# Kernel optimization log

Hardware: AMD Instinct MI355X
Metric: run time of the kernel (lower is better)

## Reference

```python
import jax, jax.numpy as jnp
import numpy as np

N_NODES = 50000
N_REL = 16
D_EMB = 128
D_HID = 128
D_OUT = 128
N_EDGES = 1600000


def _xavier(key, shape, fan_in, fan_out, dtype=jnp.float32):
    lim = float(np.sqrt(6.0 / (fan_in + fan_out)))
    return jax.random.uniform(key, shape, dtype, -lim, lim)


def setup_inputs() -> dict:
    key = jax.random.key(0)
    ks = jax.random.split(key, 10)
    edge_index = jax.random.randint(ks[0], (2, N_EDGES), 0, N_NODES, dtype=jnp.int64)
    edge_type = jax.random.randint(ks[1], (N_EDGES,), 0, N_REL, dtype=jnp.int64)
    emb = _xavier(ks[2], (N_NODES, D_EMB), N_NODES, D_EMB)
    W1 = _xavier(ks[3], (N_REL, D_EMB, D_HID), D_EMB, D_HID)
    root1 = _xavier(ks[4], (D_EMB, D_HID), D_EMB, D_HID)
    b1 = jnp.zeros((D_HID,), jnp.float32)
    W2 = _xavier(ks[5], (N_REL, D_HID, D_OUT), D_HID, D_OUT)
    root2 = _xavier(ks[6], (D_HID, D_OUT), D_HID, D_OUT)
    b2 = jnp.zeros((D_OUT,), jnp.float32)
    return {"edge_index": edge_index, "edge_type": edge_type, "emb": emb,
            "W1": W1, "root1": root1, "b1": b1,
            "W2": W2, "root2": root2, "b2": b2}


def rgcn_conv(x, edge_index, edge_type, W, W_root, b):
    """PyG RGCNConv (num_bases=None): out_i = x_i @ W_root + b + sum_r mean_{j in N_r(i)} x_j @ W_r.
    Mean-aggregate x_j per (dst, relation) first, then apply relation GEMMs (linearity)."""
    src, dst = edge_index[0], edge_index[1]
    seg = dst * N_REL + edge_type                      # [E] composite (node, rel) key
    x_src = x[src]                                     # [E, d] gather
    summed = jax.ops.segment_sum(x_src, seg, num_segments=N_NODES * N_REL)  # [N*R, d]
    cnt = jax.ops.segment_sum(jnp.ones((src.shape[0],), x.dtype), seg,
                              num_segments=N_NODES * N_REL)                 # [N*R]
    agg = summed / jnp.maximum(cnt, 1.0)[:, None]      # mean; empty (i,r) -> 0
    agg = agg.reshape(N_NODES, N_REL, x.shape[1])      # [N, R, d]
    return jnp.einsum('nrd,rdh->nh', agg, W) + x @ W_root + b


def reference(edge_index, edge_type, emb, W1, root1, b1, W2, root2, b2):
    x = emb                                            # embedding.weight: all-node lookup
    x = jax.nn.relu(rgcn_conv(x, edge_index, edge_type, W1, root1, b1))
    # dropout(p=0.5) omitted: eval-mode identity
    x = rgcn_conv(x, edge_index, edge_type, W2, root2, b2)
    return x
```

## Files before the change

kernel.cpp:

```cpp
#include <hip/hip_runtime.h>

#define N_NODES 50000
#define N_REL 16
#define D 128
#define N_SEG (N_NODES * N_REL)

typedef short bf16x8 __attribute__((ext_vector_type(8)));
typedef float f32x4 __attribute__((ext_vector_type(4)));
typedef unsigned short u16;
typedef unsigned int u32;

__device__ __forceinline__ u16 f32_to_bf16(float f) {
  u32 u = __builtin_bit_cast(u32, f);
  u32 r = (u + 0x7FFFu + ((u >> 16) & 1u)) >> 16;
  return (u16)r;
}
__device__ __forceinline__ float bf16_to_f32(u16 h) {
  u32 u = ((u32)h) << 16;
  return __builtin_bit_cast(float, u);
}

__global__ __launch_bounds__(256) void k_zero4(uint4* __restrict__ p, long long n4) {
  long long i = (long long)blockIdx.x * blockDim.x + threadIdx.x;
  long long stride = (long long)gridDim.x * blockDim.x;
  uint4 z; z.x = z.y = z.z = z.w = 0u;
  for (; i < n4; i += stride) p[i] = z;
}

__global__ __launch_bounds__(256) void k_cvt(const float* __restrict__ in,
                                             u16* __restrict__ out, long long n4) {
  long long i = (long long)blockIdx.x * blockDim.x + threadIdx.x;
  if (i >= n4) return;
  float4 v = ((const float4*)in)[i];
  u32 p0 = (u32)f32_to_bf16(v.x) | ((u32)f32_to_bf16(v.y) << 16);
  u32 p1 = (u32)f32_to_bf16(v.z) | ((u32)f32_to_bf16(v.w) << 16);
  ((u32*)out)[i * 2] = p0;
  ((u32*)out)[i * 2 + 1] = p1;
}

__global__ __launch_bounds__(256) void k_count(const int* __restrict__ dst,
                                               const int* __restrict__ rel,
                                               int* __restrict__ cnt, int E) {
  int e = blockIdx.x * blockDim.x + threadIdx.x;
  if (e < E) atomicAdd(&cnt[dst[e] * N_REL + rel[e]], 1);
}

__global__ __launch_bounds__(256) void k_bsum(const int* __restrict__ cnt,
                                              int* __restrict__ bsum, int n) {
  __shared__ int sm[256];
  int i = blockIdx.x * 256 + threadIdx.x;
  int v = (i < n) ? cnt[i] : 0;
  sm[threadIdx.x] = v;
  __syncthreads();
  for (int s = 128; s > 0; s >>= 1) {
    if (threadIdx.x < s) sm[threadIdx.x] += sm[threadIdx.x + s];
    __syncthreads();
  }
  if (threadIdx.x == 0) bsum[blockIdx.x] = sm[0];
}

__global__ __launch_bounds__(1024) void k_bscan(int* __restrict__ bsum, int nb) {
  __shared__ int sm[1024];
  __shared__ int carry;
  if (threadIdx.x == 0) carry = 0;
  __syncthreads();
  int niter = (nb + 1023) / 1024;
  for (int it = 0; it < niter; ++it) {
    int i = it * 1024 + threadIdx.x;
    int v = (i < nb) ? bsum[i] : 0;
    sm[threadIdx.x] = v;
    __syncthreads();
    for (int s = 1; s < 1024; s <<= 1) {
      int t = (threadIdx.x >= s) ? sm[threadIdx.x - s] : 0;
      __syncthreads();
      sm[threadIdx.x] += t;
      __syncthreads();
    }
    int incl = sm[threadIdx.x];
    int c = carry;
    __syncthreads();
    if (i < nb) bsum[i] = c + incl - v;
    if (threadIdx.x == 1023) carry = c + sm[1023];
    __syncthreads();
  }
}

__global__ __launch_bounds__(256) void k_off(const int* __restrict__ cnt,
                                             const int* __restrict__ bsum,
                                             int* __restrict__ off, int n) {
  __shared__ int sm[256];
  int i = blockIdx.x * 256 + threadIdx.x;
  int v = (i < n) ? cnt[i] : 0;
  sm[threadIdx.x] = v;
  __syncthreads();
  for (int s = 1; s < 256; s <<= 1) {
    int t = (threadIdx.x >= s) ? sm[threadIdx.x - s] : 0;
    __syncthreads();
    sm[threadIdx.x] += t;
    __syncthreads();
  }
  int excl = sm[threadIdx.x] - v + bsum[blockIdx.x];
  if (i < n) off[i] = excl;
  if (i == n - 1) off[n] = excl + v;
}

__global__ __launch_bounds__(256) void k_fill(const int* __restrict__ src,
                                              const int* __restrict__ dst,
                                              const int* __restrict__ rel,
                                              const int* __restrict__ off,
                                              int* __restrict__ cnt,
                                              int* __restrict__ bucket, int E) {
  int e = blockIdx.x * blockDim.x + threadIdx.x;
  if (e >= E) return;
  int seg = dst[e] * N_REL + rel[e];
  int old = atomicSub(&cnt[seg], 1);
  bucket[off[seg] + old - 1] = src[e];
}

__global__ __launch_bounds__(256) void k_wfrag(const float* __restrict__ W,
                                               u16* __restrict__ Wf, int nkb) {
  int tid = blockIdx.x * blockDim.x + threadIdx.x;
  int total = nkb * 8 * 64;
  if (tid >= total) return;
  int lane = tid & 63;
  int t = (tid >> 6) & 7;
  int kb = tid >> 9;
  int h = t * 16 + (lane & 15);
  int kbase = kb * 32 + ((lane >> 4) << 3);
  bf16x8 frag;
#pragma unroll
  for (int j = 0; j < 8; ++j) {
    int k = kbase + j;
    frag[j] = (short)f32_to_bf16(W[(size_t)(k >> 7) * (D * D) + (size_t)(k & 127) * D + h]);
  }
  *(bf16x8*)(Wf + (size_t)tid * 8) = frag;
}

template <int L>
__global__ __launch_bounds__(256) void k_layer(const int* __restrict__ off,
                                               const int* __restrict__ bucket,
                                               const u16* __restrict__ x,
                                               const u16* __restrict__ Wf,
                                               const u16* __restrict__ Rf,
                                               const float* __restrict__ bias,
                                               u16* __restrict__ outb,
                                               float* __restrict__ outf) {
  __shared__ f32x4 red[4][8][64];
  int w = threadIdx.x >> 6;
  int lane = threadIdx.x & 63;
  int node0 = blockIdx.x << 4;
  int m = lane & 15;
  int q = lane >> 4;
  int node = node0 + m;

  f32x4 acc[8];
#pragma unroll
  for (int t = 0; t < 8; ++t)
#pragma unroll
    for (int i = 0; i < 4; ++i) acc[t][i] = 0.0f;

  {
    bf16x8 a = *(const bf16x8*)(x + ((size_t)node << 7) + w * 32 + (q << 3));
    const u16* bp = Rf + ((size_t)w << 12) + ((size_t)lane << 3);
#pragma unroll
    for (int t = 0; t < 8; ++t) {
      bf16x8 b = *(const bf16x8*)(bp + t * 512);
      acc[t] = __builtin_amdgcn_mfma_f32_16x16x32_bf16(a, b, acc[t], 0, 0, 0);
    }
  }

  for (int rr = 0; rr < 4; ++rr) {
    int r = w * 4 + rr;
    int seg = (node << 4) + r;
    int o0 = off[seg];
    int o1 = off[seg + 1];

    float a0[8], a1[8], a2[8], a3[8];
#pragma unroll
    for (int j = 0; j < 8; ++j) { a0[j] = 0.f; a1[j] = 0.f; a2[j] = 0.f; a3[j] = 0.f; }

    for (int i = o0; i < o1; ++i) {
      int s = bucket[i];
      const u16* xs = x + ((size_t)s << 7) + (q << 3);
      bf16x8 v0 = *(const bf16x8*)(xs);
      bf16x8 v1 = *(const bf16x8*)(xs + 32);
      bf16x8 v2 = *(const bf16x8*)(xs + 64);
      bf16x8 v3 = *(const bf16x8*)(xs + 96);
#pragma unroll
      for (int j = 0; j < 8; ++j) {
        a0[j] += bf16_to_f32((u16)v0[j]);
        a1[j] += bf16_to_f32((u16)v1[j]);
        a2[j] += bf16_to_f32((u16)v2[j]);
        a3[j] += bf16_to_f32((u16)v3[j]);
      }
    }

    float sc = (o1 > o0) ? 1.0f / (float)(o1 - o0) : 0.0f;
    bf16x8 f0, f1, f2, f3;
#pragma unroll
    for (int j = 0; j < 8; ++j) {
      f0[j] = (short)f32_to_bf16(a0[j] * sc);
      f1[j] = (short)f32_to_bf16(a1[j] * sc);
      f2[j] = (short)f32_to_bf16(a2[j] * sc);
      f3[j] = (short)f32_to_bf16(a3[j] * sc);
    }

    const u16* bp = Wf + ((size_t)(r * 4) << 12) + ((size_t)lane << 3);
#pragma unroll
    for (int t = 0; t < 8; ++t) {
      bf16x8 b0 = *(const bf16x8*)(bp + t * 512);
      bf16x8 b1 = *(const bf16x8*)(bp + 4096 + t * 512);
      bf16x8 b2 = *(const bf16x8*)(bp + 8192 + t * 512);
      bf16x8 b3 = *(const bf16x8*)(bp + 12288 + t * 512);
      acc[t] = __builtin_amdgcn_mfma_f32_16x16x32_bf16(f0, b0, acc[t], 0, 0, 0);
      acc[t] = __builtin_amdgcn_mfma_f32_16x16x32_bf16(f1, b1, acc[t], 0, 0, 0);
      acc[t] = __builtin_amdgcn_mfma_f32_16x16x32_bf16(f2, b2, acc[t], 0, 0, 0);
      acc[t] = __builtin_amdgcn_mfma_f32_16x16x32_bf16(f3, b3, acc[t], 0, 0, 0);
    }
  }

#pragma unroll
  for (int t = 0; t < 8; ++t) red[w][t][lane] = acc[t];
  __syncthreads();

#pragma unroll
  for (int j = 0; j < 2; ++j) {
    int t = w * 2 + j;
    f32x4 s0 = red[0][t][lane];
    f32x4 s1 = red[1][t][lane];
    f32x4 s2 = red[2][t][lane];
    f32x4 s3 = red[3][t][lane];
    int h = t * 16 + m;
    float bv = bias[h];
#pragma unroll
    for (int r4 = 0; r4 < 4; ++r4) {
      int n = node0 + (q << 2) + r4;
      float v = s0[r4] + s1[r4] + s2[r4] + s3[r4] + bv;
      if (L == 1) {
        v = v > 0.0f ? v : 0.0f;
        outb[(size_t)n * D + h] = f32_to_bf16(v);
      } else {
        outf[(size_t)n * D + h] = v;
      }
    }
  }
}

extern "C" void kernel_launch(void* const* d_in, const int* in_sizes, int n_in,
                              void* d_out, int out_size, void* d_ws, size_t ws_size,
                              hipStream_t stream) {
  const int* edge_index = (const int*)d_in[0];
  const int* edge_type  = (const int*)d_in[1];
  const float* emb   = (const float*)d_in[2];
  const float* W1    = (const float*)d_in[3];
  const float* root1 = (const float*)d_in[4];
  const float* b1    = (const float*)d_in[5];
  const float* W2    = (const float*)d_in[6];
  const float* root2 = (const float*)d_in[7];
  const float* b2    = (const float*)d_in[8];
  float* out = (float*)d_out;

  int E = in_sizes[0] / 2;
  const int* src = edge_index;
  const int* dst = edge_index + E;
  int nblocks_seg = (N_SEG + 255) / 256;

  char* ws = (char*)d_ws;
  size_t off_b = 0;
  auto take = [&](size_t bytes) -> char* {
    char* p = ws + off_b;
    off_b += (bytes + 255) & ~(size_t)255;
    return p;
  };
  int*   cnt    = (int*)take((size_t)N_SEG * 4);
  int*   offs   = (int*)take((size_t)(N_SEG + 1) * 4);
  int*   bsum   = (int*)take((size_t)nblocks_seg * 4);
  int*   bucket = (int*)take((size_t)E * 4);
  u16*   embb   = (u16*)take((size_t)N_NODES * D * 2);
  u16*   x1     = (u16*)take((size_t)N_NODES * D * 2);
  u16*   Wf1    = (u16*)take((size_t)64 * 8 * 512 * 2);
  u16*   Rf1    = (u16*)take((size_t)4 * 8 * 512 * 2);
  u16*   Wf2    = (u16*)take((size_t)64 * 8 * 512 * 2);
  u16*   Rf2    = (u16*)take((size_t)4 * 8 * 512 * 2);

  int eBlocks = (E + 255) / 256;
  int layerBlocks = N_NODES / 16;

  k_zero4<<<512, 256, 0, stream>>>((uint4*)cnt, (long long)N_SEG * 4 / 16);
  k_count<<<eBlocks, 256, 0, stream>>>(dst, edge_type, cnt, E);
  k_bsum<<<nblocks_seg, 256, 0, stream>>>(cnt, bsum, N_SEG);
  k_bscan<<<1, 1024, 0, stream>>>(bsum, nblocks_seg);
  k_off<<<nblocks_seg, 256, 0, stream>>>(cnt, bsum, offs, N_SEG);
  k_fill<<<eBlocks, 256, 0, stream>>>(src, dst, edge_type, offs, cnt, bucket, E);

  k_cvt<<<((N_NODES * D / 4) + 255) / 256, 256, 0, stream>>>(emb, embb,
                                                             (long long)N_NODES * D / 4);
  k_wfrag<<<(64 * 8 * 64 + 255) / 256, 256, 0, stream>>>(W1, Wf1, 64);
  k_wfrag<<<(4 * 8 * 64 + 255) / 256, 256, 0, stream>>>(root1, Rf1, 4);
  k_wfrag<<<(64 * 8 * 64 + 255) / 256, 256, 0, stream>>>(W2, Wf2, 64);
  k_wfrag<<<(4 * 8 * 64 + 255) / 256, 256, 0, stream>>>(root2, Rf2, 4);

  k_layer<1><<<layerBlocks, 256, 0, stream>>>(offs, bucket, embb, Wf1, Rf1, b1,
                                              x1, nullptr);
  k_layer<2><<<layerBlocks, 256, 0, stream>>>(offs, bucket, x1, Wf2, Rf2, b2,
                                              nullptr, out);
}
```

Baseline: 551.2 us.

## Restructure RGCN layer: wave-per-segment gather into LDS, then per-wave output-column MFMA

New measurement: 678.8 us. 1.23x slower.

```diff
diff --git a/kernel.cpp b/kernel.cpp
--- a/kernel.cpp
+++ b/kernel.cpp
@@ -14,10 +14,6 @@
   u32 u = __builtin_bit_cast(u32, f);
   u32 r = (u + 0x7FFFu + ((u >> 16) & 1u)) >> 16;
   return (u16)r;
-}
-__device__ __forceinline__ float bf16_to_f32(u16 h) {
-  u32 u = ((u32)h) << 16;
-  return __builtin_bit_cast(float, u);
 }
 
 __global__ __launch_bounds__(256) void k_zero4(uint4* __restrict__ p, long long n4) {
@@ -137,7 +133,7 @@
 }
 
 template <int L>
-__global__ __launch_bounds__(256) void k_layer(const int* __restrict__ off,
+__global__ __launch_bounds__(512) void k_layer(const int* __restrict__ off,
                                                const int* __restrict__ bucket,
                                                const u16* __restrict__ x,
                                                const u16* __restrict__ Wf,
@@ -145,103 +141,86 @@
                                                const float* __restrict__ bias,
                                                u16* __restrict__ outb,
                                                float* __restrict__ outf) {
-  __shared__ f32x4 red[4][8][64];
-  int w = threadIdx.x >> 6;
-  int lane = threadIdx.x & 63;
+  __shared__ __align__(16) u32 agg[16 * 16 * 64];
+  __shared__ int offs_sm[257];
+  int tid = threadIdx.x;
+  int w = tid >> 6;
+  int lane = tid & 63;
   int node0 = blockIdx.x << 4;
+
+  if (tid < 257) offs_sm[tid] = off[(node0 << 4) + tid];
+  __syncthreads();
+
+  const u32* xw = (const u32*)x;
+
+  for (int k = 0; k < 32; ++k) {
+    int s = (k << 3) | w;
+    int m = s >> 4;
+    int o0 = __builtin_amdgcn_readfirstlane(offs_sm[s]);
+    int o1 = __builtin_amdgcn_readfirstlane(offs_sm[s + 1]);
+    float aL = 0.0f, aH = 0.0f;
+    int i = o0;
+    for (; i + 2 <= o1; i += 2) {
+      int e0 = __builtin_amdgcn_readfirstlane(bucket[i]);
+      int e1 = __builtin_amdgcn_readfirstlane(bucket[i + 1]);
+      u32 v0 = xw[((size_t)e0 << 6) + lane];
+      u32 v1 = xw[((size_t)e1 << 6) + lane];
+      aL += __builtin_bit_cast(float, v0 << 16);
+      aH += __builtin_bit_cast(float, v0 & 0xFFFF0000u);
+      aL += __builtin_bit_cast(float, v1 << 16);
+      aH += __builtin_bit_cast(float, v1 & 0xFFFF0000u);
+    }
+    if (i < o1) {
+      int e0 = __builtin_amdgcn_readfirstlane(bucket[i]);
+      u32 v0 = xw[((size_t)e0 << 6) + lane];
+      aL += __builtin_bit_cast(float, v0 << 16);
+      aH += __builtin_bit_cast(float, v0 & 0xFFFF0000u);
+    }
+    float sc = (o1 > o0) ? 1.0f / (float)(o1 - o0) : 0.0f;
+    u32 p = (u32)f32_to_bf16(aL * sc) | ((u32)f32_to_bf16(aH * sc) << 16);
+    agg[(s << 6) + ((((lane >> 2) ^ m) << 2) | (lane & 3))] = p;
+  }
+  __syncthreads();
+
+  int q = lane >> 4;
   int m = lane & 15;
-  int q = lane >> 4;
-  int node = node0 + m;
-
-  f32x4 acc[8];
-#pragma unroll
-  for (int t = 0; t < 8; ++t)
-#pragma unroll
-    for (int i = 0; i < 4; ++i) acc[t][i] = 0.0f;
+  const u16* aggh = (const u16*)agg;
+
+  f32x4 acc;
+#pragma unroll
+  for (int i = 0; i < 4; ++i) acc[i] = 0.0f;
 
   {
-    bf16x8 a = *(const bf16x8*)(x + ((size_t)node << 7) + w * 32 + (q << 3));
-    const u16* bp = Rf + ((size_t)w << 12) + ((size_t)lane << 3);
-#pragma unroll
-    for (int t = 0; t < 8; ++t) {
-      bf16x8 b = *(const bf16x8*)(bp + t * 512);
-      acc[t] = __builtin_amdgcn_mfma_f32_16x16x32_bf16(a, b, acc[t], 0, 0, 0);
-    }
-  }
-
-  for (int rr = 0; rr < 4; ++rr) {
-    int r = w * 4 + rr;
-    int seg = (node << 4) + r;
-    int o0 = off[seg];
-    int o1 = off[seg + 1];
-
-    float a0[8], a1[8], a2[8], a3[8];
-#pragma unroll
-    for (int j = 0; j < 8; ++j) { a0[j] = 0.f; a1[j] = 0.f; a2[j] = 0.f; a3[j] = 0.f; }
-
-    for (int i = o0; i < o1; ++i) {
-      int s = bucket[i];
-      const u16* xs = x + ((size_t)s << 7) + (q << 3);
-      bf16x8 v0 = *(const bf16x8*)(xs);
-      bf16x8 v1 = *(const bf16x8*)(xs + 32);
-      bf16x8 v2 = *(const bf16x8*)(xs + 64);
-      bf16x8 v3 = *(const bf16x8*)(xs + 96);
-#pragma unroll
-      for (int j = 0; j < 8; ++j) {
-        a0[j] += bf16_to_f32((u16)v0[j]);
-        a1[j] += bf16_to_f32((u16)v1[j]);
-        a2[j] += bf16_to_f32((u16)v2[j]);
-        a3[j] += bf16_to_f32((u16)v3[j]);
-      }
-    }
-
-    float sc = (o1 > o0) ? 1.0f / (float)(o1 - o0) : 0.0f;
-    bf16x8 f0, f1, f2, f3;
-#pragma unroll
-    for (int j = 0; j < 8; ++j) {
-      f0[j] = (short)f32_to_bf16(a0[j] * sc);
-      f1[j] = (short)f32_to_bf16(a1[j] * sc);
-      f2[j] = (short)f32_to_bf16(a2[j] * sc);
-      f3[j] = (short)f32_to_bf16(a3[j] * sc);
-    }
-
-    const u16* bp = Wf + ((size_t)(r * 4) << 12) + ((size_t)lane << 3);
-#pragma unroll
-    for (int t = 0; t < 8; ++t) {
-      bf16x8 b0 = *(const bf16x8*)(bp + t * 512);
-      bf16x8 b1 = *(const bf16x8*)(bp + 4096 + t * 512);
-      bf16x8 b2 = *(const bf16x8*)(bp + 8192 + t * 512);
-      bf16x8 b3 = *(const bf16x8*)(bp + 12288 + t * 512);
-      acc[t] = __builtin_amdgcn_mfma_f32_16x16x32_bf16(f0, b0, acc[t], 0, 0, 0);
-      acc[t] = __builtin_amdgcn_mfma_f32_16x16x32_bf16(f1, b1, acc[t], 0, 0, 0);
-      acc[t] = __builtin_amdgcn_mfma_f32_16x16x32_bf16(f2, b2, acc[t], 0, 0, 0);
-      acc[t] = __builtin_amdgcn_mfma_f32_16x16x32_bf16(f3, b3, acc[t], 0, 0, 0);
-    }
-  }
-
-#pragma unroll
-  for (int t = 0; t < 8; ++t) red[w][t][lane] = acc[t];
-  __syncthreads();
-
-#pragma unroll
-  for (int j = 0; j < 2; ++j) {
-    int t = w * 2 + j;
-    f32x4 s0 = red[0][t][lane];
-    f32x4 s1 = red[1][t][lane];
-    f32x4 s2 = red[2][t][lane];
-    f32x4 s3 = red[3][t][lane];
-    int h = t * 16 + m;
-    float bv = bias[h];
-#pragma unroll
-    for (int r4 = 0; r4 < 4; ++r4) {
-      int n = node0 + (q << 2) + r4;
-      float v = s0[r4] + s1[r4] + s2[r4] + s3[r4] + bv;
-      if (L == 1) {
-        v = v > 0.0f ? v : 0.0f;
-        outb[(size_t)n * D + h] = f32_to_bf16(v);
-      } else {
-        outf[(size_t)n * D + h] = v;
-      }
+    const u16* xr = x + ((size_t)(node0 + m) << 7) + (q << 3);
+#pragma unroll
+    for (int kb = 0; kb < 4; ++kb) {
+      bf16x8 a = *(const bf16x8*)(xr + kb * 32);
+      bf16x8 b = *(const bf16x8*)(Rf + ((((kb << 3) + w) << 9) | (lane << 3)));
+      acc = __builtin_amdgcn_mfma_f32_16x16x32_bf16(a, b, acc, 0, 0, 0);
+    }
+  }
+
+  for (int r = 0; r < 16; ++r) {
+#pragma unroll
+    for (int kb = 0; kb < 4; ++kb) {
+      int c = ((kb << 2) | q) ^ m;
+      bf16x8 a = *(const bf16x8*)(aggh + ((((m << 4) | r) << 7) | (c << 3)));
+      bf16x8 b = *(const bf16x8*)(Wf + (((((r << 2) | kb) << 3) + w) << 9) + (lane << 3));
+      acc = __builtin_amdgcn_mfma_f32_16x16x32_bf16(a, b, acc, 0, 0, 0);
+    }
+  }
+
+  int h = (w << 4) + m;
+  float bv = bias[h];
+#pragma unroll
+  for (int j = 0; j < 4; ++j) {
+    int n = node0 + (q << 2) + j;
+    float v = acc[j] + bv;
+    if (L == 1) {
+      v = v > 0.0f ? v : 0.0f;
+      outb[(size_t)n * D + h] = f32_to_bf16(v);
+    } else {
+      outf[(size_t)n * D + h] = v;
     }
   }
 }
@@ -300,8 +279,8 @@
   k_wfrag<<<(64 * 8 * 64 + 255) / 256, 256, 0, stream>>>(W2, Wf2, 64);
   k_wfrag<<<(4 * 8 * 64 + 255) / 256, 256, 0, stream>>>(root2, Rf2, 4);
 
-  k_layer<1><<<layerBlocks, 256, 0, stream>>>(offs, bucket, embb, Wf1, Rf1, b1,
+  k_layer<1><<<layerBlocks, 512, 0, stream>>>(offs, bucket, embb, Wf1, Rf1, b1,
                                               x1, nullptr);
-  k_layer<2><<<layerBlocks, 256, 0, stream>>>(offs, bucket, x1, Wf2, Rf2, b2,
+  k_layer<2><<<layerBlocks, 512, 0, stream>>>(offs, bucket, x1, Wf2, Rf2, b2,
                                               nullptr, out);
 }
```

## Process two 16-node tiles per block to reuse weight fragments; merge prep kernels

Applied to the files above, without the earlier changes.

Measured after the change: 626.3 us. 13.6% more time.

```diff
diff --git a/kernel.cpp b/kernel.cpp
--- a/kernel.cpp
+++ b/kernel.cpp
@@ -25,17 +25,6 @@
   long long stride = (long long)gridDim.x * blockDim.x;
   uint4 z; z.x = z.y = z.z = z.w = 0u;
   for (; i < n4; i += stride) p[i] = z;
-}
-
-__global__ __launch_bounds__(256) void k_cvt(const float* __restrict__ in,
-                                             u16* __restrict__ out, long long n4) {
-  long long i = (long long)blockIdx.x * blockDim.x + threadIdx.x;
-  if (i >= n4) return;
-  float4 v = ((const float4*)in)[i];
-  u32 p0 = (u32)f32_to_bf16(v.x) | ((u32)f32_to_bf16(v.y) << 16);
-  u32 p1 = (u32)f32_to_bf16(v.z) | ((u32)f32_to_bf16(v.w) << 16);
-  ((u32*)out)[i * 2] = p0;
-  ((u32*)out)[i * 2 + 1] = p1;
 }
 
 __global__ __launch_bounds__(256) void k_count(const int* __restrict__ dst,
@@ -117,11 +106,8 @@
   bucket[off[seg] + old - 1] = src[e];
 }
 
-__global__ __launch_bounds__(256) void k_wfrag(const float* __restrict__ W,
-                                               u16* __restrict__ Wf, int nkb) {
-  int tid = blockIdx.x * blockDim.x + threadIdx.x;
-  int total = nkb * 8 * 64;
-  if (tid >= total) return;
+__device__ __forceinline__ void wfrag_one(const float* __restrict__ W,
+                                          u16* __restrict__ Wf, int tid) {
   int lane = tid & 63;
   int t = (tid >> 6) & 7;
   int kb = tid >> 9;
@@ -136,73 +122,149 @@
   *(bf16x8*)(Wf + (size_t)tid * 8) = frag;
 }
 
+#define CVT_N4 (N_NODES * D / 4)
+#define WF_T (64 * 8 * 64)
+#define RF_T (4 * 8 * 64)
+#define PREP_TOTAL (CVT_N4 + 2 * WF_T + 2 * RF_T)
+
+__global__ __launch_bounds__(256) void k_prep(const float* __restrict__ emb,
+                                              u16* __restrict__ embb,
+                                              const float* __restrict__ W1,
+                                              u16* __restrict__ Wf1,
+                                              const float* __restrict__ W2,
+                                              u16* __restrict__ Wf2,
+                                              const float* __restrict__ R1,
+                                              u16* __restrict__ Rf1,
+                                              const float* __restrict__ R2,
+                                              u16* __restrict__ Rf2) {
+  int tid = blockIdx.x * blockDim.x + threadIdx.x;
+  if (tid < CVT_N4) {
+    float4 v = ((const float4*)emb)[tid];
+    u32 p0 = (u32)f32_to_bf16(v.x) | ((u32)f32_to_bf16(v.y) << 16);
+    u32 p1 = (u32)f32_to_bf16(v.z) | ((u32)f32_to_bf16(v.w) << 16);
+    ((u32*)embb)[tid * 2] = p0;
+    ((u32*)embb)[tid * 2 + 1] = p1;
+    return;
+  }
+  int u = tid - CVT_N4;
+  if (u < WF_T) { wfrag_one(W1, Wf1, u); return; }
+  u -= WF_T;
+  if (u < WF_T) { wfrag_one(W2, Wf2, u); return; }
+  u -= WF_T;
+  if (u < RF_T) { wfrag_one(R1, Rf1, u); return; }
+  u -= RF_T;
+  if (u < RF_T) { wfrag_one(R2, Rf2, u); return; }
+}
+
 template <int L>
-__global__ __launch_bounds__(256) void k_layer(const int* __restrict__ off,
-                                               const int* __restrict__ bucket,
-                                               const u16* __restrict__ x,
-                                               const u16* __restrict__ Wf,
-                                               const u16* __restrict__ Rf,
-                                               const float* __restrict__ bias,
-                                               u16* __restrict__ outb,
-                                               float* __restrict__ outf) {
+__global__ __launch_bounds__(256, 3) void k_layer(const int* __restrict__ off,
+                                                  const int* __restrict__ bucket,
+                                                  const u16* __restrict__ x,
+                                                  const u16* __restrict__ Wf,
+                                                  const u16* __restrict__ Rf,
+                                                  const float* __restrict__ bias,
+                                                  u16* __restrict__ outb,
+                                                  float* __restrict__ outf) {
   __shared__ f32x4 red[4][8][64];
   int w = threadIdx.x >> 6;
   int lane = threadIdx.x & 63;
-  int node0 = blockIdx.x << 4;
+  int node0 = blockIdx.x << 5;
   int m = lane & 15;
   int q = lane >> 4;
-  int node = node0 + m;
-
-  f32x4 acc[8];
+  int nA = node0 + m;
+  bool hasB = (node0 + 16) < N_NODES;
+  int nB = hasB ? (node0 + 16 + m) : nA;
+
+  f32x4 acc0[8], acc1[8];
 #pragma unroll
   for (int t = 0; t < 8; ++t)
 #pragma unroll
-    for (int i = 0; i < 4; ++i) acc[t][i] = 0.0f;
+    for (int i = 0; i < 4; ++i) { acc0[t][i] = 0.0f; acc1[t][i] = 0.0f; }
 
   {
-    bf16x8 a = *(const bf16x8*)(x + ((size_t)node << 7) + w * 32 + (q << 3));
+    bf16x8 aA = *(const bf16x8*)(x + ((size_t)nA << 7) + w * 32 + (q << 3));
+    bf16x8 aB = *(const bf16x8*)(x + ((size_t)nB << 7) + w * 32 + (q << 3));
     const u16* bp = Rf + ((size_t)w << 12) + ((size_t)lane << 3);
 #pragma unroll
     for (int t = 0; t < 8; ++t) {
       bf16x8 b = *(const bf16x8*)(bp + t * 512);
-      acc[t] = __builtin_amdgcn_mfma_f32_16x16x32_bf16(a, b, acc[t], 0, 0, 0);
-    }
+      acc0[t] = __builtin_amdgcn_mfma_f32_16x16x32_bf16(aA, b, acc0[t], 0, 0, 0);
+      acc1[t] = __builtin_amdgcn_mfma_f32_16x16x32_bf16(aB, b, acc1[t], 0, 0, 0);
+    }
+  }
+
+  int oA[5], oB[5];
+  {
+    int sgA = (nA << 4) + (w << 2);
+    int sgB = (nB << 4) + (w << 2);
+#pragma unroll
+    for (int t = 0; t < 5; ++t) { oA[t] = off[sgA + t]; oB[t] = off[sgB + t]; }
   }
 
   for (int rr = 0; rr < 4; ++rr) {
-    int r = w * 4 + rr;
-    int seg = (node << 4) + r;
-    int o0 = off[seg];
-    int o1 = off[seg + 1];
-
-    float a0[8], a1[8], a2[8], a3[8];
-#pragma unroll
-    for (int j = 0; j < 8; ++j) { a0[j] = 0.f; a1[j] = 0.f; a2[j] = 0.f; a3[j] = 0.f; }
-
-    for (int i = o0; i < o1; ++i) {
-      int s = bucket[i];
-      const u16* xs = x + ((size_t)s << 7) + (q << 3);
-      bf16x8 v0 = *(const bf16x8*)(xs);
-      bf16x8 v1 = *(const bf16x8*)(xs + 32);
-      bf16x8 v2 = *(const bf16x8*)(xs + 64);
-      bf16x8 v3 = *(const bf16x8*)(xs + 96);
+    int r = (w << 2) + rr;
+
+    bf16x8 f0, f1, f2, f3;
+    bf16x8 g0, g1, g2, g3;
+
+    {
+      float a0[8], a1[8], a2[8], a3[8];
+#pragma unroll
+      for (int j = 0; j < 8; ++j) { a0[j] = 0.f; a1[j] = 0.f; a2[j] = 0.f; a3[j] = 0.f; }
+      int o0 = oA[rr], o1 = oA[rr + 1];
+      for (int i = o0; i < o1; ++i) {
+        int s = bucket[i];
+        const u16* xs = x + ((size_t)s << 7) + (q << 3);
+        bf16x8 v0 = *(const bf16x8*)(xs);
+        bf16x8 v1 = *(const bf16x8*)(xs + 32);
+        bf16x8 v2 = *(const bf16x8*)(xs + 64);
+        bf16x8 v3 = *(const bf16x8*)(xs + 96);
+#pragma unroll
+        for (int j = 0; j < 8; ++j) {
+          a0[j] += bf16_to_f32((u16)v0[j]);
+          a1[j] += bf16_to_f32((u16)v1[j]);
+          a2[j] += bf16_to_f32((u16)v2[j]);
+          a3[j] += bf16_to_f32((u16)v3[j]);
+        }
+      }
+      float sc = (o1 > o0) ? 1.0f / (float)(o1 - o0) : 0.0f;
 #pragma unroll
       for (int j = 0; j < 8; ++j) {
-        a0[j] += bf16_to_f32((u16)v0[j]);
-        a1[j] += bf16_to_f32((u16)v1[j]);
-        a2[j] += bf16_to_f32((u16)v2[j]);
-        a3[j] += bf16_to_f32((u16)v3[j]);
-      }
-    }
-
-    float sc = (o1 > o0) ? 1.0f / (float)(o1 - o0) : 0.0f;
-    bf16x8 f0, f1, f2, f3;
-#pragma unroll
-    for (int j = 0; j < 8; ++j) {
-      f0[j] = (short)f32_to_bf16(a0[j] * sc);
-      f1[j] = (short)f32_to_bf16(a1[j] * sc);
-      f2[j] = (short)f32_to_bf16(a2[j] * sc);
-      f3[j] = (short)f32_to_bf16(a3[j] * sc);
+        f0[j] = (short)f32_to_bf16(a0[j] * sc);
+        f1[j] = (short)f32_to_bf16(a1[j] * sc);
+        f2[j] = (short)f32_to_bf16(a2[j] * sc);
+        f3[j] = (short)f32_to_bf16(a3[j] * sc);
+      }
+    }
+
+    {
+      float a0[8], a1[8], a2[8], a3[8];
+#pragma unroll
+      for (int j = 0; j < 8; ++j) { a0[j] = 0.f; a1[j] = 0.f; a2[j] = 0.f; a3[j] = 0.f; }
+      int o0 = oB[rr], o1 = hasB ? oB[rr + 1] : oB[rr];
+      for (int i = o0; i < o1; ++i) {
+        int s = bucket[i];
+        const u16* xs = x + ((size_t)s << 7) + (q << 3);
+        bf16x8 v0 = *(const bf16x8*)(xs);
+        bf16x8 v1 = *(const bf16x8*)(xs + 32);
+        bf16x8 v2 = *(const bf16x8*)(xs + 64);
+        bf16x8 v3 = *(const bf16x8*)(xs + 96);
+#pragma unroll
+        for (int j = 0; j < 8; ++j) {
+          a0[j] += bf16_to_f32((u16)v0[j]);
+          a1[j] += bf16_to_f32((u16)v1[j]);
+          a2[j] += bf16_to_f32((u16)v2[j]);
+          a3[j] += bf16_to_f32((u16)v3[j]);
+        }
+      }
+      float sc = (o1 > o0) ? 1.0f / (float)(o1 - o0) : 0.0f;
+#pragma unroll
+      for (int j = 0; j < 8; ++j) {
+        g0[j] = (short)f32_to_bf16(a0[j] * sc);
+        g1[j] = (short)f32_to_bf16(a1[j] * sc);
+        g2[j] = (short)f32_to_bf16(a2[j] * sc);
+        g3[j] = (short)f32_to_bf16(a3[j] * sc);
+      }
     }
 
     const u16* bp = Wf + ((size_t)(r * 4) << 12) + ((size_t)lane << 3);
@@ -212,17 +274,20 @@
       bf16x8 b1 = *(const bf16x8*)(bp + 4096 + t * 512);
       bf16x8 b2 = *(const bf16x8*)(bp + 8192 + t * 512);
       bf16x8 b3 = *(const bf16x8*)(bp + 12288 + t * 512);
-      acc[t] = __builtin_amdgcn_mfma_f32_16x16x32_bf16(f0, b0, acc[t], 0, 0, 0);
-      acc[t] = __builtin_amdgcn_mfma_f32_16x16x32_bf16(f1, b1, acc[t], 0, 0, 0);
-      acc[t] = __builtin_amdgcn_mfma_f32_16x16x32_bf16(f2, b2, acc[t], 0, 0, 0);
-      acc[t] = __builtin_amdgcn_mfma_f32_16x16x32_bf16(f3, b3, acc[t], 0, 0, 0);
-    }
-  }
-
-#pragma unroll
-  for (int t = 0; t < 8; ++t) red[w][t][lane] = acc[t];
-  __syncthreads();
-
+      acc0[t] = __builtin_amdgcn_mfma_f32_16x16x32_bf16(f0, b0, acc0[t], 0, 0, 0);
+      acc1[t] = __builtin_amdgcn_mfma_f32_16x16x32_bf16(g0, b0, acc1[t], 0, 0, 0);
+      acc0[t] = __builtin_amdgcn_mfma_f32_16x16x32_bf16(f1, b1, acc0[t], 0, 0, 0);
+      acc1[t] = __builtin_amdgcn_mfma_f32_16x16x32_bf16(g1, b1, acc1[t], 0, 0, 0);
+      acc0[t] = __builtin_amdgcn_mfma_f32_16x16x32_bf16(f2, b2, acc0[t], 0, 0, 0);
+      acc1[t] = __builtin_amdgcn_mfma_f32_16x16x32_bf16(g2, b2, acc1[t], 0, 0, 0);
+      acc0[t] = __builtin_amdgcn_mfma_f32_16x16x32_bf16(f3, b3, acc0[t], 0, 0, 0);
+      acc1[t] = __builtin_amdgcn_mfma_f32_16x16x32_bf16(g3, b3, acc1[t], 0, 0, 0);
+    }
+  }
+
+#pragma unroll
+  for (int t = 0; t < 8; ++t) red[w][t][lane] = acc0[t];
+  __syncthreads();
 #pragma unroll
   for (int j = 0; j < 2; ++j) {
     int t = w * 2 + j;
@@ -241,6 +306,34 @@
         outb[(size_t)n * D + h] = f32_to_bf16(v);
       } else {
         outf[(size_t)n * D + h] = v;
+      }
+    }
+  }
+  __syncthreads();
+
+#pragma unroll
+  for (int t = 0; t < 8; ++t) red[w][t][lane] = acc1[t];
+  __syncthreads();
+  if (hasB) {
+#pragma unroll
+    for (int j = 0; j < 2; ++j) {
+      int t = w * 2 + j;
+      f32x4 s0 = red[0][t][lane];
+      f32x4 s1 = red[1][t][lane];
+      f32x4 s2 = red[2][t][lane];
+      f32x4 s3 = red[3][t][lane];
+      int h = t * 16 + m;
+      float bv = bias[h];
+#pragma unroll
+      for (int r4 = 0; r4 < 4; ++r4) {
+        int n = node0 + 16 + (q << 2) + r4;
+        float v = s0[r4] + s1[r4] + s2[r4] + s3[r4] + bv;
+        if (L == 1) {
+          v = v > 0.0f ? v : 0.0f;
+          outb[(size_t)n * D + h] = f32_to_bf16(v);
+        } else {
+          outf[(size_t)n * D + h] = v;
+        }
       }
     }
   }
@@ -284,7 +377,7 @@
   u16*   Rf2    = (u16*)take((size_t)4 * 8 * 512 * 2);
 
   int eBlocks = (E + 255) / 256;
-  int layerBlocks = N_NODES / 16;
+  int layerBlocks = (N_NODES + 31) / 32;
 
   k_zero4<<<512, 256, 0, stream>>>((uint4*)cnt, (long long)N_SEG * 4 / 16);
   k_count<<<eBlocks, 256, 0, stream>>>(dst, edge_type, cnt, E);
@@ -293,12 +386,8 @@
   k_off<<<nblocks_seg, 256, 0, stream>>>(cnt, bsum, offs, N_SEG);
   k_fill<<<eBlocks, 256, 0, stream>>>(src, dst, edge_type, offs, cnt, bucket, E);
 
-  k_cvt<<<((N_NODES * D / 4) + 255) / 256, 256, 0, stream>>>(emb, embb,
-                                                             (long long)N_NODES * D / 4);
-  k_wfrag<<<(64 * 8 * 64 + 255) / 256, 256, 0, stream>>>(W1, Wf1, 64);
-  k_wfrag<<<(4 * 8 * 64 + 255) / 256, 256, 0, stream>>>(root1, Rf1, 4);
-  k_wfrag<<<(64 * 8 * 64 + 255) / 256, 256, 0, stream>>>(W2, Wf2, 64);
-  k_wfrag<<<(4 * 8 * 64 + 255) / 256, 256, 0, stream>>>(root2, Rf2, 4);
+  k_prep<<<(PREP_TOTAL + 255) / 256, 256, 0, stream>>>(emb, embb, W1, Wf1, W2, Wf2,
+                                                       root1, Rf1, root2, Rf2);
 
   k_layer<1><<<layerBlocks, 256, 0, stream>>>(offs, bucket, embb, Wf1, Rf1, b1,
                                               x1, nullptr);
```

## Stage relation weights in LDS per block, give each wave its own nodes

Applied to the files above, without the earlier changes.

Result: slower. 742.1 us (+34.6%).

```diff
diff --git a/kernel.cpp b/kernel.cpp
--- a/kernel.cpp
+++ b/kernel.cpp
@@ -25,17 +25,6 @@
   long long stride = (long long)gridDim.x * blockDim.x;
   uint4 z; z.x = z.y = z.z = z.w = 0u;
   for (; i < n4; i += stride) p[i] = z;
-}
-
-__global__ __launch_bounds__(256) void k_cvt(const float* __restrict__ in,
-                                             u16* __restrict__ out, long long n4) {
-  long long i = (long long)blockIdx.x * blockDim.x + threadIdx.x;
-  if (i >= n4) return;
-  float4 v = ((const float4*)in)[i];
-  u32 p0 = (u32)f32_to_bf16(v.x) | ((u32)f32_to_bf16(v.y) << 16);
-  u32 p1 = (u32)f32_to_bf16(v.z) | ((u32)f32_to_bf16(v.w) << 16);
-  ((u32*)out)[i * 2] = p0;
-  ((u32*)out)[i * 2 + 1] = p1;
 }
 
 __global__ __launch_bounds__(256) void k_count(const int* __restrict__ dst,
@@ -117,11 +106,8 @@
   bucket[off[seg] + old - 1] = src[e];
 }
 
-__global__ __launch_bounds__(256) void k_wfrag(const float* __restrict__ W,
-                                               u16* __restrict__ Wf, int nkb) {
-  int tid = blockIdx.x * blockDim.x + threadIdx.x;
-  int total = nkb * 8 * 64;
-  if (tid >= total) return;
+__device__ __forceinline__ void wfrag_one(const float* __restrict__ W,
+                                          u16* __restrict__ Wf, int tid) {
   int lane = tid & 63;
   int t = (tid >> 6) & 7;
   int kb = tid >> 9;
@@ -134,6 +120,40 @@
     frag[j] = (short)f32_to_bf16(W[(size_t)(k >> 7) * (D * D) + (size_t)(k & 127) * D + h]);
   }
   *(bf16x8*)(Wf + (size_t)tid * 8) = frag;
+}
+
+#define CVT_N4 (N_NODES * D / 4)
+#define WF_T (64 * 8 * 64)
+#define RF_T (4 * 8 * 64)
+#define PREP_TOTAL (CVT_N4 + 2 * WF_T + 2 * RF_T)
+
+__global__ __launch_bounds__(256) void k_prep(const float* __restrict__ emb,
+                                              u16* __restrict__ embb,
+                                              const float* __restrict__ W1,
+                                              u16* __restrict__ Wf1,
+                                              const float* __restrict__ W2,
+                                              u16* __restrict__ Wf2,
+                                              const float* __restrict__ R1,
+                                              u16* __restrict__ Rf1,
+                                              const float* __restrict__ R2,
+                                              u16* __restrict__ Rf2) {
+  int tid = blockIdx.x * blockDim.x + threadIdx.x;
+  if (tid < CVT_N4) {
+    float4 v = ((const float4*)emb)[tid];
+    u32 p0 = (u32)f32_to_bf16(v.x) | ((u32)f32_to_bf16(v.y) << 16);
+    u32 p1 = (u32)f32_to_bf16(v.z) | ((u32)f32_to_bf16(v.w) << 16);
+    ((u32*)embb)[tid * 2] = p0;
+    ((u32*)embb)[tid * 2 + 1] = p1;
+    return;
+  }
+  int u = tid - CVT_N4;
+  if (u < WF_T) { wfrag_one(W1, Wf1, u); return; }
+  u -= WF_T;
+  if (u < WF_T) { wfrag_one(W2, Wf2, u); return; }
+  u -= WF_T;
+  if (u < RF_T) { wfrag_one(R1, Rf1, u); return; }
+  u -= RF_T;
+  if (u < RF_T) { wfrag_one(R2, Rf2, u); return; }
 }
 
 template <int L>
@@ -145,13 +165,15 @@
                                                const float* __restrict__ bias,
                                                u16* __restrict__ outb,
                                                float* __restrict__ outf) {
-  __shared__ f32x4 red[4][8][64];
-  int w = threadIdx.x >> 6;
-  int lane = threadIdx.x & 63;
-  int node0 = blockIdx.x << 4;
+  __shared__ __align__(16) u16 bsm[16384];
+  int tid = threadIdx.x;
+  int w = tid >> 6;
+  int lane = tid & 63;
+  int node0 = blockIdx.x << 6;
   int m = lane & 15;
   int q = lane >> 4;
-  int node = node0 + m;
+  int node = node0 + (w << 4) + m;
+  int nodec = node < N_NODES ? node : (N_NODES - 1);
 
   f32x4 acc[8];
 #pragma unroll
@@ -159,59 +181,62 @@
 #pragma unroll
     for (int i = 0; i < 4; ++i) acc[t][i] = 0.0f;
 
-  {
-    bf16x8 a = *(const bf16x8*)(x + ((size_t)node << 7) + w * 32 + (q << 3));
-    const u16* bp = Rf + ((size_t)w << 12) + ((size_t)lane << 3);
+  for (int r = 0; r < 17; ++r) {
+    bf16x8 f0, f1, f2, f3;
+    if (r == 16) {
+      const u16* xr = x + ((size_t)nodec << 7) + (q << 3);
+      f0 = *(const bf16x8*)(xr);
+      f1 = *(const bf16x8*)(xr + 32);
+      f2 = *(const bf16x8*)(xr + 64);
+      f3 = *(const bf16x8*)(xr + 96);
+    } else {
+      int seg = (nodec << 4) + r;
+      int o0 = off[seg];
+      int o1 = off[seg + 1];
+      float a0[8], a1[8], a2[8], a3[8];
+#pragma unroll
+      for (int j = 0; j < 8; ++j) { a0[j] = 0.f; a1[j] = 0.f; a2[j] = 0.f; a3[j] = 0.f; }
+      for (int i = o0; i < o1; ++i) {
+        int s = bucket[i];
+        const u16* xs = x + ((size_t)s << 7) + (q << 3);
+        bf16x8 v0 = *(const bf16x8*)(xs);
+        bf16x8 v1 = *(const bf16x8*)(xs + 32);
+        bf16x8 v2 = *(const bf16x8*)(xs + 64);
+        bf16x8 v3 = *(const bf16x8*)(xs + 96);
+#pragma unroll
+        for (int j = 0; j < 8; ++j) {
+          a0[j] += bf16_to_f32((u16)v0[j]);
+          a1[j] += bf16_to_f32((u16)v1[j]);
+          a2[j] += bf16_to_f32((u16)v2[j]);
+          a3[j] += bf16_to_f32((u16)v3[j]);
+        }
+      }
+      float sc = (o1 > o0) ? 1.0f / (float)(o1 - o0) : 0.0f;
+#pragma unroll
+      for (int j = 0; j < 8; ++j) {
+        f0[j] = (short)f32_to_bf16(a0[j] * sc);
+        f1[j] = (short)f32_to_bf16(a1[j] * sc);
+        f2[j] = (short)f32_to_bf16(a2[j] * sc);
+        f3[j] = (short)f32_to_bf16(a3[j] * sc);
+      }
+    }
+
+    __syncthreads();
+    {
+      const uint4* bsrc = (const uint4*)((r < 16) ? (Wf + ((size_t)r << 14)) : Rf);
+#pragma unroll
+      for (int i = 0; i < 8; ++i)
+        ((uint4*)bsm)[(i << 8) | tid] = bsrc[(i << 8) | tid];
+    }
+    __syncthreads();
+
 #pragma unroll
     for (int t = 0; t < 8; ++t) {
-      bf16x8 b = *(const bf16x8*)(bp + t * 512);
-      acc[t] = __builtin_amdgcn_mfma_f32_16x16x32_bf16(a, b, acc[t], 0, 0, 0);
-    }
-  }
-
-  for (int rr = 0; rr < 4; ++rr) {
-    int r = w * 4 + rr;
-    int seg = (node << 4) + r;
-    int o0 = off[seg];
-    int o1 = off[seg + 1];
-
-    float a0[8], a1[8], a2[8], a3[8];
-#pragma unroll
-    for (int j = 0; j < 8; ++j) { a0[j] = 0.f; a1[j] = 0.f; a2[j] = 0.f; a3[j] = 0.f; }
-
-    for (int i = o0; i < o1; ++i) {
-      int s = bucket[i];
-      const u16* xs = x + ((size_t)s << 7) + (q << 3);
-      bf16x8 v0 = *(const bf16x8*)(xs);
-      bf16x8 v1 = *(const bf16x8*)(xs + 32);
-      bf16x8 v2 = *(const bf16x8*)(xs + 64);
-      bf16x8 v3 = *(const bf16x8*)(xs + 96);
-#pragma unroll
-      for (int j = 0; j < 8; ++j) {
-        a0[j] += bf16_to_f32((u16)v0[j]);
-        a1[j] += bf16_to_f32((u16)v1[j]);
-        a2[j] += bf16_to_f32((u16)v2[j]);
-        a3[j] += bf16_to_f32((u16)v3[j]);
-      }
-    }
-
-    float sc = (o1 > o0) ? 1.0f / (float)(o1 - o0) : 0.0f;
-    bf16x8 f0, f1, f2, f3;
-#pragma unroll
-    for (int j = 0; j < 8; ++j) {
-      f0[j] = (short)f32_to_bf16(a0[j] * sc);
-      f1[j] = (short)f32_to_bf16(a1[j] * sc);
-      f2[j] = (short)f32_to_bf16(a2[j] * sc);
-      f3[j] = (short)f32_to_bf16(a3[j] * sc);
-    }
-
-    const u16* bp = Wf + ((size_t)(r * 4) << 12) + ((size_t)lane << 3);
-#pragma unroll
-    for (int t = 0; t < 8; ++t) {
-      bf16x8 b0 = *(const bf16x8*)(bp + t * 512);
-      bf16x8 b1 = *(const bf16x8*)(bp + 4096 + t * 512);
-      bf16x8 b2 = *(const bf16x8*)(bp + 8192 + t * 512);
-      bf16x8 b3 = *(const bf16x8*)(bp + 12288 + t * 512);
+      const u16* bp = bsm + (t << 9) + (lane << 3);
+      bf16x8 b0 = *(const bf16x8*)(bp);
+      bf16x8 b1 = *(const bf16x8*)(bp + 4096);
+      bf16x8 b2 = *(const bf16x8*)(bp + 8192);
+      bf16x8 b3 = *(const bf16x8*)(bp + 12288);
       acc[t] = __builtin_amdgcn_mfma_f32_16x16x32_bf16(f0, b0, acc[t], 0, 0, 0);
       acc[t] = __builtin_amdgcn_mfma_f32_16x16x32_bf16(f1, b1, acc[t], 0, 0, 0);
       acc[t] = __builtin_amdgcn_mfma_f32_16x16x32_bf16(f2, b2, acc[t], 0, 0, 0);
@@ -220,27 +245,20 @@
   }
 
 #pragma unroll
-  for (int t = 0; t < 8; ++t) red[w][t][lane] = acc[t];
-  __syncthreads();
-
-#pragma unroll
-  for (int j = 0; j < 2; ++j) {
-    int t = w * 2 + j;
-    f32x4 s0 = red[0][t][lane];
-    f32x4 s1 = red[1][t][lane];
-    f32x4 s2 = red[2][t][lane];
-    f32x4 s3 = red[3][t][lane];
-    int h = t * 16 + m;
+  for (int t = 0; t < 8; ++t) {
+    int h = (t << 4) + m;
     float bv = bias[h];
 #pragma unroll
-    for (int r4 = 0; r4 < 4; ++r4) {
-      int n = node0 + (q << 2) + r4;
-      float v = s0[r4] + s1[r4] + s2[r4] + s3[r4] + bv;
-      if (L == 1) {
-        v = v > 0.0f ? v : 0.0f;
-        outb[(size_t)n * D + h] = f32_to_bf16(v);
-      } else {
-        outf[(size_t)n * D + h] = v;
+    for (int j = 0; j < 4; ++j) {
+      int n = node0 + (w << 4) + (q << 2) + j;
+      if (n < N_NODES) {
+        float v = acc[t][j] + bv;
+        if (L == 1) {
+          v = v > 0.0f ? v : 0.0f;
+          outb[(size_t)n * D + h] = f32_to_bf16(v);
+        } else {
+          outf[(size_t)n * D + h] = v;
+        }
       }
     }
   }
@@ -284,7 +302,7 @@
   u16*   Rf2    = (u16*)take((size_t)4 * 8 * 512 * 2);
 
   int eBlocks = (E + 255) / 256;
-  int layerBlocks = N_NODES / 16;
+  int layerBlocks = (N_NODES + 63) / 64;
 
   k_zero4<<<512, 256, 0, stream>>>((uint4*)cnt, (long long)N_SEG * 4 / 16);
   k_count<<<eBlocks, 256, 0, stream>>>(dst, edge_type, cnt, E);
@@ -293,12 +311,8 @@
   k_off<<<nblocks_seg, 256, 0, stream>>>(cnt, bsum, offs, N_SEG);
   k_fill<<<eBlocks, 256, 0, stream>>>(src, dst, edge_type, offs, cnt, bucket, E);
 
-  k_cvt<<<((N_NODES * D / 4) + 255) / 256, 256, 0, stream>>>(emb, embb,
-                                                             (long long)N_NODES * D / 4);
-  k_wfrag<<<(64 * 8 * 64 + 255) / 256, 256, 0, stream>>>(W1, Wf1, 64);
-  k_wfrag<<<(4 * 8 * 64 + 255) / 256, 256, 0, stream>>>(root1, Rf1, 4);
-  k_wfrag<<<(64 * 8 * 64 + 255) / 256, 256, 0, stream>>>(W2, Wf2, 64);
-  k_wfrag<<<(4 * 8 * 64 + 255) / 256, 256, 0, stream>>>(root2, Rf2, 4);
+  k_prep<<<(PREP_TOTAL + 255) / 256, 256, 0, stream>>>(emb, embb, W1, Wf1, W2, Wf2,
+                                                       root1, Rf1, root2, Rf2);
 
   k_layer<1><<<layerBlocks, 256, 0, stream>>>(offs, bucket, embb, Wf1, Rf1, b1,
                                               x1, nullptr);
```
